# Performance work log

Measured on AMD Instinct MI355X. Metric: run time of the kernel, lower is better.

## Reference

```python
import jax, jax.numpy as jnp
import numpy as np

B, C, H = 16, 64, 128
W_SCALE = 0.05  # keep softmax logits in a sane range


def conv1x1_relu(x, w, b):
    # x: [B,C,H,W], w: [O,C] (1x1 conv kernel squeezed), b: [O]
    y = jnp.einsum('bchw,oc->bohw', x, w) + b[None, :, None, None]
    return jax.nn.relu(y)


def setup_inputs() -> dict:
    key = jax.random.key(0)
    ks = jax.random.split(key, 10)
    inp = {
        'x': jax.random.normal(ks[0], (B, C, H, H), dtype=jnp.float32),
        'att': jax.random.normal(ks[1], (B, C, H, H), dtype=jnp.float32),
    }
    for i in range(4):
        inp[f'w{i}'] = jax.random.normal(ks[2 + 2 * i], (C, C), dtype=jnp.float32) * W_SCALE
        inp[f'b{i}'] = jax.random.normal(ks[3 + 2 * i], (C,), dtype=jnp.float32) * W_SCALE
    return inp


def reference(x, att, w0, b0, w1, b1, w2, b2, w3, b3):
    bs, c, h, w = x.shape
    query = conv1x1_relu(x, w0, b0)    # [B,C,H,W]
    key_ = conv1x1_relu(att, w1, b1)   # [B,C,H,W]
    value = conv1x1_relu(x, w2, b2)    # [B,C,H,W]
    kt = jnp.swapaxes(key_, -2, -1)    # [B,C,W,H]
    attn1 = jax.nn.softmax(jnp.matmul(query, kt), axis=-1)  # [B,C,H,H]
    attn2 = jax.nn.softmax(jnp.matmul(kt, query), axis=-1)  # [B,C,W,W]
    out = jnp.matmul(jnp.matmul(attn1, value), attn2)       # [B,C,H,W]
    out = conv1x1_relu(out, w3, b3)
    return out.reshape(bs, -1, h, h)
```

## Files before the change

kernel.cpp:

```cpp
#include <hip/hip_runtime.h>
#include <stdint.h>

#define NB   16
#define NCH  64
#define HH   128
#define NPOS (HH*HH)

typedef short bf16x8 __attribute__((ext_vector_type(8)));
typedef float f32x4  __attribute__((ext_vector_type(4)));

__device__ __forceinline__ unsigned short f2bf(float f){
  unsigned int u = __float_as_uint(f);
  u += 0x7FFFu + ((u>>16)&1u);
  return (unsigned short)(u>>16);
}
__device__ __forceinline__ unsigned int pk2(float a, float b){
  return (unsigned int)f2bf(a) | ((unsigned int)f2bf(b)<<16);
}

__device__ __forceinline__ int swz(int row, int cb){
  return cb ^ (((row & 7) ^ ((row >> 3) & 7)) << 4);
}

__global__ __launch_bounds__(256) void rc_conv_in(
    const float* __restrict__ x, const float* __restrict__ att,
    const float* __restrict__ w0, const float* __restrict__ b0,
    const float* __restrict__ w1, const float* __restrict__ b1,
    const float* __restrict__ w2, const float* __restrict__ b2,
    unsigned short* __restrict__ Qb, unsigned short* __restrict__ Kb,
    unsigned short* __restrict__ Vb)
{
  __shared__ char smem[49664];
  char* Xs  = smem;
  char* WsA = smem + 32768;
  char* WsB = smem + 40960;
  float* biasA = (float*)(smem + 49152);
  float* biasB = (float*)(smem + 49408);

  const int tid = threadIdx.x;
  const int m  = blockIdx.z;
  const int b  = blockIdx.y;
  const int pblock = blockIdx.x * 256;
  const float* src = m ? att : x;
  const float* wA  = m ? w1 : w0;
  const float* bA  = m ? b1 : b0;

  {
    int o = tid >> 2, c0 = (tid & 3) * 16;
    const float4* wr = (const float4*)(wA + o*64 + c0);
    float4 f0 = wr[0], f1 = wr[1], f2v = wr[2], f3 = wr[3];
    uint4 pa, pb;
    pa.x = pk2(f0.x,f0.y);  pa.y = pk2(f0.z,f0.w);
    pa.z = pk2(f1.x,f1.y);  pa.w = pk2(f1.z,f1.w);
    pb.x = pk2(f2v.x,f2v.y); pb.y = pk2(f2v.z,f2v.w);
    pb.z = pk2(f3.x,f3.y);  pb.w = pk2(f3.z,f3.w);
    *(uint4*)(WsA + o*128 + swz(o, c0*2))      = pa;
    *(uint4*)(WsA + o*128 + swz(o, c0*2 + 16)) = pb;
    if (m == 0){
      const float4* wr2 = (const float4*)(w2 + o*64 + c0);
      float4 g0 = wr2[0], g1 = wr2[1], g2 = wr2[2], g3 = wr2[3];
      uint4 qa, qb;
      qa.x = pk2(g0.x,g0.y); qa.y = pk2(g0.z,g0.w);
      qa.z = pk2(g1.x,g1.y); qa.w = pk2(g1.z,g1.w);
      qb.x = pk2(g2.x,g2.y); qb.y = pk2(g2.z,g2.w);
      qb.z = pk2(g3.x,g3.y); qb.w = pk2(g3.z,g3.w);
      *(uint4*)(WsB + o*128 + swz(o, c0*2))      = qa;
      *(uint4*)(WsB + o*128 + swz(o, c0*2 + 16)) = qb;
    }
  }
  if (tid < 64){
    biasA[tid] = bA[tid];
    if (m == 0) biasB[tid] = b2[tid];
  }

  const float* S = src + (size_t)b*NCH*NPOS + pblock;
  #pragma unroll
  for (int it=0; it<4; ++it){
    int unit = tid + 256*it;
    int q  = unit >> 6;
    int p4 = (unit & 63) << 2;
    float4 r0 = *(const float4*)(S + (size_t)(4*q+0)*NPOS + p4);
    float4 r1 = *(const float4*)(S + (size_t)(4*q+1)*NPOS + p4);
    float4 r2 = *(const float4*)(S + (size_t)(4*q+2)*NPOS + p4);
    float4 r3 = *(const float4*)(S + (size_t)(4*q+3)*NPOS + p4);
    const float* c0 = (const float*)&r0;
    const float* c1 = (const float*)&r1;
    const float* c2 = (const float*)&r2;
    const float* c3 = (const float*)&r3;
    #pragma unroll
    for (int u=0; u<4; ++u){
      uint2 pk;
      pk.x = pk2(c0[u], c1[u]);
      pk.y = pk2(c2[u], c3[u]);
      *(uint2*)(Xs + (p4+u)*128 + swz(p4+u, q*8)) = pk;
    }
  }
  __syncthreads();

  const int w = tid>>6, l = tid&63, lq = l>>4, lm = l&15;
  bf16x8 aQ[2], aV[2] = {};
  {
    int orow = 16*w + lm;
    aQ[0] = *(const bf16x8*)(WsA + orow*128 + swz(orow,      lq*16));
    aQ[1] = *(const bf16x8*)(WsA + orow*128 + swz(orow, 64 + lq*16));
    if (m == 0){
      aV[0] = *(const bf16x8*)(WsB + orow*128 + swz(orow,      lq*16));
      aV[1] = *(const bf16x8*)(WsB + orow*128 + swz(orow, 64 + lq*16));
    }
  }
  float bQv[4], bVv[4];
  #pragma unroll
  for (int r4=0;r4<4;r4++){
    int o = 16*w + 4*lq + r4;
    bQv[r4] = biasA[o];
    bVv[r4] = (m==0) ? biasB[o] : 0.f;
  }
  unsigned short* dA = (m ? Kb : Qb) + (size_t)b*NCH*NPOS;
  unsigned short* dB = Vb + (size_t)b*NCH*NPOS;

  #pragma unroll
  for (int pt=0; pt<16; ++pt){
    int prow = pt*16 + lm;
    bf16x8 bx0 = *(const bf16x8*)(Xs + prow*128 + swz(prow,      lq*16));
    bf16x8 bx1 = *(const bf16x8*)(Xs + prow*128 + swz(prow, 64 + lq*16));
    f32x4 accQ = (f32x4){0.f,0.f,0.f,0.f};
    accQ = __builtin_amdgcn_mfma_f32_16x16x32_bf16(aQ[0], bx0, accQ, 0,0,0);
    accQ = __builtin_amdgcn_mfma_f32_16x16x32_bf16(aQ[1], bx1, accQ, 0,0,0);
    int p = pblock + pt*16 + lm;
    #pragma unroll
    for (int r4=0;r4<4;r4++){
      int o = 16*w + 4*lq + r4;
      dA[(size_t)o*NPOS + p] = f2bf(fmaxf(accQ[r4] + bQv[r4], 0.f));
    }
    if (m == 0){
      f32x4 accV = (f32x4){0.f,0.f,0.f,0.f};
      accV = __builtin_amdgcn_mfma_f32_16x16x32_bf16(aV[0], bx0, accV, 0,0,0);
      accV = __builtin_amdgcn_mfma_f32_16x16x32_bf16(aV[1], bx1, accV, 0,0,0);
      #pragma unroll
      for (int r4=0;r4<4;r4++){
        int o = 16*w + 4*lq + r4;
        dB[(size_t)o*NPOS + p] = f2bf(fmaxf(accV[r4] + bVv[r4], 0.f));
      }
    }
  }
}

__global__ __launch_bounds__(512) void rc_attention_mfma(
    const unsigned short* __restrict__ Qb, const unsigned short* __restrict__ Kb,
    const unsigned short* __restrict__ Vb, unsigned short* __restrict__ Pb)
{
  extern __shared__ char lds[];
  char* B0 = lds;
  char* B1 = lds + 32768;
  char* B2 = lds + 65536;
  char* B3 = lds + 98304;
  const int tid = threadIdx.x;
  const int l  = tid & 63;
  const int w  = tid >> 6;
  const int lq = l >> 4;
  const int lm = l & 15;
  const size_t gbase = (size_t)blockIdx.x * NPOS;

  uint4 vreg[4];
  #pragma unroll
  for (int i=0;i<4;i++)
    vreg[i] = *(const uint4*)(Vb + gbase + (size_t)(tid + 512*i)*8);

  #pragma unroll
  for (int i=0;i<4;i++){
    int e = (tid + 512*i)*8;
    int row = e >> 7, col = e & 127;
    uint4 q = *(const uint4*)(Qb + gbase + e);
    uint4 k = *(const uint4*)(Kb + gbase + e);
    *(uint4*)(B0 + row*256 + swz(row, col*2)) = q;
    *(uint4*)(B1 + row*256 + swz(row, col*2)) = k;
    unsigned int qd[4] = {q.x,q.y,q.z,q.w};
    unsigned int kd[4] = {k.x,k.y,k.z,k.w};
    #pragma unroll
    for (int u=0;u<8;u++){
      unsigned short qe = (unsigned short)(qd[u>>1] >> (16*(u&1)));
      unsigned short ke = (unsigned short)(kd[u>>1] >> (16*(u&1)));
      int tr = col + u;
      *(unsigned short*)(B2 + tr*256 + swz(tr, row*2)) = qe;
      *(unsigned short*)(B3 + tr*256 + swz(tr, row*2)) = ke;
    }
  }
  __syncthreads();

  f32x4 acc1[8];
  #pragma unroll
  for (int t=0;t<8;t++) acc1[t] = (f32x4){0.f,0.f,0.f,0.f};
  {
    bf16x8 bq[4];
    #pragma unroll
    for (int kk=0;kk<4;kk++){
      int r = 16*w + lm;
      bq[kk] = *(const bf16x8*)(B0 + r*256 + swz(r, kk*64 + lq*16));
    }
    #pragma unroll
    for (int kk=0;kk<4;kk++){
      #pragma unroll
      for (int jt=0;jt<8;jt++){
        int jr = jt*16 + lm;
        bf16x8 ak = *(const bf16x8*)(B1 + jr*256 + swz(jr, kk*64 + lq*16));
        acc1[jt] = __builtin_amdgcn_mfma_f32_16x16x32_bf16(ak, bq[kk], acc1[jt], 0,0,0);
      }
    }
  }
  unsigned int a1p[8][2];
  {
    float mx = -1e30f;
    #pragma unroll
    for (int t=0;t<8;t++)
      mx = fmaxf(mx, fmaxf(fmaxf(acc1[t][0], acc1[t][1]), fmaxf(acc1[t][2], acc1[t][3])));
    mx = fmaxf(mx, __shfl_xor(mx, 16));
    mx = fmaxf(mx, __shfl_xor(mx, 32));
    float sum = 0.f;
    #pragma unroll
    for (int t=0;t<8;t++){
      #pragma unroll
      for (int r4=0;r4<4;r4++){ float e = __expf(acc1[t][r4] - mx); acc1[t][r4] = e; sum += e; }
    }
    sum += __shfl_xor(sum, 16);
    sum += __shfl_xor(sum, 32);
    float inv = 1.f/sum;
    #pragma unroll
    for (int t=0;t<8;t++){
      a1p[t][0] = pk2(acc1[t][0]*inv, acc1[t][1]*inv);
      a1p[t][1] = pk2(acc1[t][2]*inv, acc1[t][3]*inv);
    }
  }

  f32x4 acc2[8];
  #pragma unroll
  for (int t=0;t<8;t++) acc2[t] = (f32x4){0.f,0.f,0.f,0.f};
  {
    bf16x8 akt[4];
    #pragma unroll
    for (int kk=0;kk<4;kk++){
      int ir = 16*w + lm;
      akt[kk] = *(const bf16x8*)(B3 + ir*256 + swz(ir, kk*64 + lq*16));
    }
    #pragma unroll
    for (int kk=0;kk<4;kk++){
      #pragma unroll
      for (int ct=0;ct<8;ct++){
        int jr = ct*16 + lm;
        bf16x8 bqt = *(const bf16x8*)(B2 + jr*256 + swz(jr, kk*64 + lq*16));
        acc2[ct] = __builtin_amdgcn_mfma_f32_16x16x32_bf16(akt[kk], bqt, acc2[ct], 0,0,0);
      }
    }
  }
  unsigned int a2p[8][2];
  {
    float m0=-1e30f, m1=-1e30f, m2=-1e30f, m3=-1e30f;
    #pragma unroll
    for (int t=0;t<8;t++){
      m0 = fmaxf(m0, acc2[t][0]); m1 = fmaxf(m1, acc2[t][1]);
      m2 = fmaxf(m2, acc2[t][2]); m3 = fmaxf(m3, acc2[t][3]);
    }
    #pragma unroll
    for (int d=1; d<16; d<<=1){
      m0 = fmaxf(m0, __shfl_xor(m0,d)); m1 = fmaxf(m1, __shfl_xor(m1,d));
      m2 = fmaxf(m2, __shfl_xor(m2,d)); m3 = fmaxf(m3, __shfl_xor(m3,d));
    }
    float s0=0.f, s1=0.f, s2=0.f, s3=0.f;
    #pragma unroll
    for (int t=0;t<8;t++){
      float e0 = __expf(acc2[t][0]-m0); acc2[t][0]=e0; s0 += e0;
      float e1 = __expf(acc2[t][1]-m1); acc2[t][1]=e1; s1 += e1;
      float e2 = __expf(acc2[t][2]-m2); acc2[t][2]=e2; s2 += e2;
      float e3 = __expf(acc2[t][3]-m3); acc2[t][3]=e3; s3 += e3;
    }
    #pragma unroll
    for (int d=1; d<16; d<<=1){
      s0 += __shfl_xor(s0,d); s1 += __shfl_xor(s1,d);
      s2 += __shfl_xor(s2,d); s3 += __shfl_xor(s3,d);
    }
    float i0=1.f/s0, i1=1.f/s1, i2=1.f/s2, i3=1.f/s3;
    #pragma unroll
    for (int t=0;t<8;t++){
      a2p[t][0] = pk2(acc2[t][0]*i0, acc2[t][1]*i1);
      a2p[t][1] = pk2(acc2[t][2]*i2, acc2[t][3]*i3);
    }
  }

  __syncthreads();

  {
    int r = 16*w + lm;
    #pragma unroll
    for (int t=0;t<8;t++)
      *(uint2*)(B3 + r*256 + swz(r, t*32 + lq*8)) = make_uint2(a1p[t][0], a1p[t][1]);
  }
  #pragma unroll
  for (int t=0;t<8;t++){
    int jr = t*16 + lm;
    *(uint2*)(B2 + jr*256 + swz(jr, 32*w + lq*8)) = make_uint2(a2p[t][0], a2p[t][1]);
  }
  #pragma unroll
  for (int i=0;i<4;i++){
    int e = (tid + 512*i)*8;
    int row = e>>7, col = e&127;
    unsigned int vd[4] = {vreg[i].x, vreg[i].y, vreg[i].z, vreg[i].w};
    #pragma unroll
    for (int u=0;u<8;u++){
      unsigned short ve = (unsigned short)(vd[u>>1] >> (16*(u&1)));
      int tr = col + u;
      *(unsigned short*)(B1 + tr*256 + swz(tr, row*2)) = ve;
    }
  }
  __syncthreads();

  f32x4 acc3[8];
  #pragma unroll
  for (int t=0;t<8;t++) acc3[t] = (f32x4){0.f,0.f,0.f,0.f};
  {
    bf16x8 av[4];
    #pragma unroll
    for (int kk=0;kk<4;kk++){
      int jr = 16*w + lm;
      av[kk] = *(const bf16x8*)(B1 + jr*256 + swz(jr, kk*64 + lq*16));
    }
    #pragma unroll
    for (int kk=0;kk<4;kk++){
      #pragma unroll
      for (int rt=0;rt<8;rt++){
        int rr = rt*16 + lm;
        bf16x8 ba = *(const bf16x8*)(B3 + rr*256 + swz(rr, kk*64 + lq*16));
        acc3[rt] = __builtin_amdgcn_mfma_f32_16x16x32_bf16(av[kk], ba, acc3[rt], 0,0,0);
      }
    }
  }
  #pragma unroll
  for (int rt=0;rt<8;rt++){
    int rr = rt*16 + lm;
    unsigned int p0 = pk2(acc3[rt][0], acc3[rt][1]);
    unsigned int p1 = pk2(acc3[rt][2], acc3[rt][3]);
    *(uint2*)(B0 + rr*256 + swz(rr, 32*w + lq*8)) = make_uint2(p0, p1);
  }
  __syncthreads();

  f32x4 acc4[8];
  #pragma unroll
  for (int t=0;t<8;t++) acc4[t] = (f32x4){0.f,0.f,0.f,0.f};
  {
    bf16x8 am[4];
    #pragma unroll
    for (int kk=0;kk<4;kk++){
      int rr = 16*w + lm;
      am[kk] = *(const bf16x8*)(B0 + rr*256 + swz(rr, kk*64 + lq*16));
    }
    #pragma unroll
    for (int kk=0;kk<4;kk++){
      #pragma unroll
      for (int ct=0;ct<8;ct++){
        int jr = ct*16 + lm;
        bf16x8 ba2 = *(const bf16x8*)(B2 + jr*256 + swz(jr, kk*64 + lq*16));
        acc4[ct] = __builtin_amdgcn_mfma_f32_16x16x32_bf16(am[kk], ba2, acc4[ct], 0,0,0);
      }
    }
  }
  unsigned short* pout = Pb + gbase;
  #pragma unroll
  for (int ct=0;ct<8;ct++){
    #pragma unroll
    for (int r4=0;r4<4;r4++){
      int rr = 16*w + lq*4 + r4;
      pout[rr*HH + ct*16 + lm] = f2bf(acc4[ct][r4]);
    }
  }
}

__global__ __launch_bounds__(256) void rc_conv_out(
    const unsigned short* __restrict__ Pb, const float* __restrict__ w3,
    const float* __restrict__ b3, float* __restrict__ out)
{
  __shared__ char smem[41216];
  char* Xs = smem;
  char* Ws = smem + 32768;
  float* bias = (float*)(smem + 40960);

  const int tid = threadIdx.x;
  const int b  = blockIdx.y;
  const int pblock = blockIdx.x * 256;

  {
    int o = tid >> 2, c0 = (tid & 3) * 16;
    const float4* wr = (const float4*)(w3 + o*64 + c0);
    float4 f0 = wr[0], f1 = wr[1], f2v = wr[2], f3 = wr[3];
    uint4 pa, pb;
    pa.x = pk2(f0.x,f0.y);  pa.y = pk2(f0.z,f0.w);
    pa.z = pk2(f1.x,f1.y);  pa.w = pk2(f1.z,f1.w);
    pb.x = pk2(f2v.x,f2v.y); pb.y = pk2(f2v.z,f2v.w);
    pb.z = pk2(f3.x,f3.y);  pb.w = pk2(f3.z,f3.w);
    *(uint4*)(Ws + o*128 + swz(o, c0*2))      = pa;
    *(uint4*)(Ws + o*128 + swz(o, c0*2 + 16)) = pb;
  }
  if (tid < 64) bias[tid] = b3[tid];

  const unsigned short* S = Pb + (size_t)b*NCH*NPOS + pblock;
  #pragma unroll
  for (int it=0; it<4; ++it){
    int unit = tid + 256*it;
    int q  = unit >> 6;
    int p4 = (unit & 63) << 2;
    uint2 r0 = *(const uint2*)(S + (size_t)(4*q+0)*NPOS + p4);
    uint2 r1 = *(const uint2*)(S + (size_t)(4*q+1)*NPOS + p4);
    uint2 r2 = *(const uint2*)(S + (size_t)(4*q+2)*NPOS + p4);
    uint2 r3 = *(const uint2*)(S + (size_t)(4*q+3)*NPOS + p4);
    const unsigned short* u0 = (const unsigned short*)&r0;
    const unsigned short* u1 = (const unsigned short*)&r1;
    const unsigned short* u2 = (const unsigned short*)&r2;
    const unsigned short* u3 = (const unsigned short*)&r3;
    #pragma unroll
    for (int u=0; u<4; ++u){
      uint2 pk;
      pk.x = (unsigned int)u0[u] | ((unsigned int)u1[u]<<16);
      pk.y = (unsigned int)u2[u] | ((unsigned int)u3[u]<<16);
      *(uint2*)(Xs + (p4+u)*128 + swz(p4+u, q*8)) = pk;
    }
  }
  __syncthreads();

  const int w = tid>>6, l = tid&63, lq = l>>4, lm = l&15;
  bf16x8 aW[2];
  {
    int orow = 16*w + lm;
    aW[0] = *(const bf16x8*)(Ws + orow*128 + swz(orow,      lq*16));
    aW[1] = *(const bf16x8*)(Ws + orow*128 + swz(orow, 64 + lq*16));
  }
  float bv[4];
  #pragma unroll
  for (int r4=0;r4<4;r4++) bv[r4] = bias[16*w + 4*lq + r4];

  float* dst = out + (size_t)b*NCH*NPOS;
  #pragma unroll
  for (int pt=0; pt<16; ++pt){
    int prow = pt*16 + lm;
    bf16x8 bx0 = *(const bf16x8*)(Xs + prow*128 + swz(prow,      lq*16));
    bf16x8 bx1 = *(const bf16x8*)(Xs + prow*128 + swz(prow, 64 + lq*16));
    f32x4 acc = (f32x4){0.f,0.f,0.f,0.f};
    acc = __builtin_amdgcn_mfma_f32_16x16x32_bf16(aW[0], bx0, acc, 0,0,0);
    acc = __builtin_amdgcn_mfma_f32_16x16x32_bf16(aW[1], bx1, acc, 0,0,0);
    int p = pblock + pt*16 + lm;
    #pragma unroll
    for (int r4=0;r4<4;r4++){
      int o = 16*w + 4*lq + r4;
      dst[(size_t)o*NPOS + p] = fmaxf(acc[r4] + bv[r4], 0.f);
    }
  }
}

extern "C" void kernel_launch(void* const* d_in, const int* in_sizes, int n_in,
                              void* d_out, int out_size, void* d_ws, size_t ws_size,
                              hipStream_t stream)
{
  const float* x   = (const float*)d_in[0];
  const float* att = (const float*)d_in[1];
  const float* w0  = (const float*)d_in[2]; const float* b0 = (const float*)d_in[3];
  const float* w1  = (const float*)d_in[4]; const float* b1 = (const float*)d_in[5];
  const float* w2  = (const float*)d_in[6]; const float* b2 = (const float*)d_in[7];
  const float* w3  = (const float*)d_in[8]; const float* b3 = (const float*)d_in[9];

  const size_t NM = (size_t)NB*NCH*NPOS;
  unsigned short* Qb = (unsigned short*)d_ws;
  unsigned short* Kb = Qb + NM;
  unsigned short* Vb = Kb + NM;
  unsigned short* Pb = Vb + NM;
  float* out = (float*)d_out;

  (void)hipFuncSetAttribute((const void*)rc_attention_mfma,
                            hipFuncAttributeMaxDynamicSharedMemorySize, 131072);

  rc_conv_in<<<dim3(64, NB, 2), 256, 0, stream>>>(x, att, w0,b0, w1,b1, w2,b2,
                                                  Qb, Kb, Vb);

  rc_attention_mfma<<<dim3(NB*NCH), 512, 131072, stream>>>(Qb, Kb, Vb, Pb);

  rc_conv_out<<<dim3(64, NB), 256, 0, stream>>>(Pb, w3, b3, out);
}
```

Before: 125.5 us.

## Halve conv tile size, batch loads, and stage conv_in outputs through LDS

Both 1x1 conv kernels now handle 128 positions per block instead of 256 and launch twice as many blocks. They set launch-bound occupancy hints and issue all global loads before converting into LDS. In conv_in, results are accumulated for all tiles, then transposed through swizzled LDS so each thread writes 16-byte vectors instead of scattered 2-byte stores. This targets poor store coalescing and low occupancy, at the cost of extra barriers and more accumulator registers.

```diff
diff --git a/kernel.cpp b/kernel.cpp
--- a/kernel.cpp
+++ b/kernel.cpp
@@ -22,7 +22,7 @@
   return cb ^ (((row & 7) ^ ((row >> 3) & 7)) << 4);
 }
 
-__global__ __launch_bounds__(256) void rc_conv_in(
+__global__ __launch_bounds__(256, 4) void rc_conv_in(
     const float* __restrict__ x, const float* __restrict__ att,
     const float* __restrict__ w0, const float* __restrict__ b0,
     const float* __restrict__ w1, const float* __restrict__ b1,
@@ -30,17 +30,17 @@
     unsigned short* __restrict__ Qb, unsigned short* __restrict__ Kb,
     unsigned short* __restrict__ Vb)
 {
-  __shared__ char smem[49664];
+  __shared__ char smem[33280];
   char* Xs  = smem;
-  char* WsA = smem + 32768;
-  char* WsB = smem + 40960;
-  float* biasA = (float*)(smem + 49152);
-  float* biasB = (float*)(smem + 49408);
+  char* WsA = smem + 16384;
+  char* WsB = smem + 24576;
+  float* biasA = (float*)(smem + 32768);
+  float* biasB = (float*)(smem + 33024);
 
   const int tid = threadIdx.x;
   const int m  = blockIdx.z;
   const int b  = blockIdx.y;
-  const int pblock = blockIdx.x * 256;
+  const int pblock = blockIdx.x * 128;
   const float* src = m ? att : x;
   const float* wA  = m ? w1 : w0;
   const float* bA  = m ? b1 : b0;
@@ -74,19 +74,25 @@
   }
 
   const float* S = src + (size_t)b*NCH*NPOS + pblock;
-  #pragma unroll
-  for (int it=0; it<4; ++it){
-    int unit = tid + 256*it;
-    int q  = unit >> 6;
-    int p4 = (unit & 63) << 2;
-    float4 r0 = *(const float4*)(S + (size_t)(4*q+0)*NPOS + p4);
-    float4 r1 = *(const float4*)(S + (size_t)(4*q+1)*NPOS + p4);
-    float4 r2 = *(const float4*)(S + (size_t)(4*q+2)*NPOS + p4);
-    float4 r3 = *(const float4*)(S + (size_t)(4*q+3)*NPOS + p4);
-    const float* c0 = (const float*)&r0;
-    const float* c1 = (const float*)&r1;
-    const float* c2 = (const float*)&r2;
-    const float* c3 = (const float*)&r3;
+  float4 xr[2][4];
+  #pragma unroll
+  for (int g=0; g<2; ++g){
+    int unit = tid + 256*g;
+    int q  = unit >> 5;
+    int p4 = (unit & 31) << 2;
+    #pragma unroll
+    for (int j=0;j<4;j++)
+      xr[g][j] = *(const float4*)(S + (size_t)(4*q+j)*NPOS + p4);
+  }
+  #pragma unroll
+  for (int g=0; g<2; ++g){
+    int unit = tid + 256*g;
+    int q  = unit >> 5;
+    int p4 = (unit & 31) << 2;
+    const float* c0 = (const float*)&xr[g][0];
+    const float* c1 = (const float*)&xr[g][1];
+    const float* c2 = (const float*)&xr[g][2];
+    const float* c3 = (const float*)&xr[g][3];
     #pragma unroll
     for (int u=0; u<4; ++u){
       uint2 pk;
@@ -115,32 +121,69 @@
     bQv[r4] = biasA[o];
     bVv[r4] = (m==0) ? biasB[o] : 0.f;
   }
-  unsigned short* dA = (m ? Kb : Qb) + (size_t)b*NCH*NPOS;
-  unsigned short* dB = Vb + (size_t)b*NCH*NPOS;
-
-  #pragma unroll
-  for (int pt=0; pt<16; ++pt){
+
+  f32x4 accQ[8], accV[8];
+  #pragma unroll
+  for (int pt=0;pt<8;pt++){ accQ[pt]=(f32x4){0,0,0,0}; accV[pt]=(f32x4){0,0,0,0}; }
+  #pragma unroll
+  for (int pt=0; pt<8; ++pt){
     int prow = pt*16 + lm;
     bf16x8 bx0 = *(const bf16x8*)(Xs + prow*128 + swz(prow,      lq*16));
     bf16x8 bx1 = *(const bf16x8*)(Xs + prow*128 + swz(prow, 64 + lq*16));
-    f32x4 accQ = (f32x4){0.f,0.f,0.f,0.f};
-    accQ = __builtin_amdgcn_mfma_f32_16x16x32_bf16(aQ[0], bx0, accQ, 0,0,0);
-    accQ = __builtin_amdgcn_mfma_f32_16x16x32_bf16(aQ[1], bx1, accQ, 0,0,0);
-    int p = pblock + pt*16 + lm;
+    accQ[pt] = __builtin_amdgcn_mfma_f32_16x16x32_bf16(aQ[0], bx0, accQ[pt], 0,0,0);
+    accQ[pt] = __builtin_amdgcn_mfma_f32_16x16x32_bf16(aQ[1], bx1, accQ[pt], 0,0,0);
+    if (m == 0){
+      accV[pt] = __builtin_amdgcn_mfma_f32_16x16x32_bf16(aV[0], bx0, accV[pt], 0,0,0);
+      accV[pt] = __builtin_amdgcn_mfma_f32_16x16x32_bf16(aV[1], bx1, accV[pt], 0,0,0);
+    }
+  }
+
+  unsigned short* dA = (m ? Kb : Qb) + (size_t)b*NCH*NPOS;
+  unsigned short* dB = Vb + (size_t)b*NCH*NPOS;
+  const int skw = 32*((4*w + lq) & 7);
+
+  __syncthreads();
+  #pragma unroll
+  for (int pt=0; pt<8; ++pt){
     #pragma unroll
     for (int r4=0;r4<4;r4++){
       int o = 16*w + 4*lq + r4;
-      dA[(size_t)o*NPOS + p] = f2bf(fmaxf(accQ[r4] + bQv[r4], 0.f));
-    }
-    if (m == 0){
-      f32x4 accV = (f32x4){0.f,0.f,0.f,0.f};
-      accV = __builtin_amdgcn_mfma_f32_16x16x32_bf16(aV[0], bx0, accV, 0,0,0);
-      accV = __builtin_amdgcn_mfma_f32_16x16x32_bf16(aV[1], bx1, accV, 0,0,0);
+      int p = pt*16 + lm;
+      *(unsigned short*)(Xs + o*256 + ((2*p + skw) & 255)) =
+          f2bf(fmaxf(accQ[pt][r4] + bQv[r4], 0.f));
+    }
+  }
+  __syncthreads();
+  {
+    int o = tid >> 2, jj = tid & 3;
+    int sk2 = 32*((o>>2)&7);
+    #pragma unroll
+    for (int i=0;i<4;i++){
+      int j = i*4 + jj;
+      uint4 v = *(const uint4*)(Xs + o*256 + ((j*16 + sk2) & 255));
+      *(uint4*)(dA + (size_t)o*NPOS + pblock + j*8) = v;
+    }
+  }
+  if (m == 0){
+    __syncthreads();
+    #pragma unroll
+    for (int pt=0; pt<8; ++pt){
       #pragma unroll
       for (int r4=0;r4<4;r4++){
         int o = 16*w + 4*lq + r4;
-        dB[(size_t)o*NPOS + p] = f2bf(fmaxf(accV[r4] + bVv[r4], 0.f));
+        int p = pt*16 + lm;
+        *(unsigned short*)(Xs + o*256 + ((2*p + skw) & 255)) =
+            f2bf(fmaxf(accV[pt][r4] + bVv[r4], 0.f));
       }
+    }
+    __syncthreads();
+    int o = tid >> 2, jj = tid & 3;
+    int sk2 = 32*((o>>2)&7);
+    #pragma unroll
+    for (int i=0;i<4;i++){
+      int j = i*4 + jj;
+      uint4 v = *(const uint4*)(Xs + o*256 + ((j*16 + sk2) & 255));
+      *(uint4*)(dB + (size_t)o*NPOS + pblock + j*8) = v;
     }
   }
 }
@@ -372,18 +415,18 @@
   }
 }
 
-__global__ __launch_bounds__(256) void rc_conv_out(
+__global__ __launch_bounds__(256, 6) void rc_conv_out(
     const unsigned short* __restrict__ Pb, const float* __restrict__ w3,
     const float* __restrict__ b3, float* __restrict__ out)
 {
-  __shared__ char smem[41216];
+  __shared__ char smem[24832];
   char* Xs = smem;
-  char* Ws = smem + 32768;
-  float* bias = (float*)(smem + 40960);
+  char* Ws = smem + 16384;
+  float* bias = (float*)(smem + 24576);
 
   const int tid = threadIdx.x;
   const int b  = blockIdx.y;
-  const int pblock = blockIdx.x * 256;
+  const int pblock = blockIdx.x * 128;
 
   {
     int o = tid >> 2, c0 = (tid & 3) * 16;
@@ -400,24 +443,30 @@
   if (tid < 64) bias[tid] = b3[tid];
 
   const unsigned short* S = Pb + (size_t)b*NCH*NPOS + pblock;
-  #pragma unroll
-  for (int it=0; it<4; ++it){
-    int unit = tid + 256*it;
-    int q  = unit >> 6;
-    int p4 = (unit & 63) << 2;
-    uint2 r0 = *(const uint2*)(S + (size_t)(4*q+0)*NPOS + p4);
-    uint2 r1 = *(const uint2*)(S + (size_t)(4*q+1)*NPOS + p4);
-    uint2 r2 = *(const uint2*)(S + (size_t)(4*q+2)*NPOS + p4);
-    uint2 r3 = *(const uint2*)(S + (size_t)(4*q+3)*NPOS + p4);
-    const unsigned short* u0 = (const unsigned short*)&r0;
-    const unsigned short* u1 = (const unsigned short*)&r1;
-    const unsigned short* u2 = (const unsigned short*)&r2;
-    const unsigned short* u3 = (const unsigned short*)&r3;
+  uint2 pr[2][4];
+  #pragma unroll
+  for (int g=0; g<2; ++g){
+    int unit = tid + 256*g;
+    int q  = unit >> 5;
+    int p4 = (unit & 31) << 2;
+    #pragma unroll
+    for (int j=0;j<4;j++)
+      pr[g][j] = *(const uint2*)(S + (size_t)(4*q+j)*NPOS + p4);
+  }
+  #pragma unroll
+  for (int g=0; g<2; ++g){
+    int unit = tid + 256*g;
+    int q  = unit >> 5;
+    int p4 = (unit & 31) << 2;
+    const unsigned short* e0 = (const unsigned short*)&pr[g][0];
+    const unsigned short* e1 = (const unsigned short*)&pr[g][1];
+    const unsigned short* e2 = (const unsigned short*)&pr[g][2];
+    const unsigned short* e3 = (const unsigned short*)&pr[g][3];
     #pragma unroll
     for (int u=0; u<4; ++u){
       uint2 pk;
-      pk.x = (unsigned int)u0[u] | ((unsigned int)u1[u]<<16);
-      pk.y = (unsigned int)u2[u] | ((unsigned int)u3[u]<<16);
+      pk.x = (unsigned int)e0[u] | ((unsigned int)e1[u]<<16);
+      pk.y = (unsigned int)e2[u] | ((unsigned int)e3[u]<<16);
       *(uint2*)(Xs + (p4+u)*128 + swz(p4+u, q*8)) = pk;
     }
   }
@@ -436,7 +485,7 @@
 
   float* dst = out + (size_t)b*NCH*NPOS;
   #pragma unroll
-  for (int pt=0; pt<16; ++pt){
+  for (int pt=0; pt<8; ++pt){
     int prow = pt*16 + lm;
     bf16x8 bx0 = *(const bf16x8*)(Xs + prow*128 + swz(prow,      lq*16));
     bf16x8 bx1 = *(const bf16x8*)(Xs + prow*128 + swz(prow, 64 + lq*16));
@@ -473,10 +522,10 @@
   (void)hipFuncSetAttribute((const void*)rc_attention_mfma,
                             hipFuncAttributeMaxDynamicSharedMemorySize, 131072);
 
-  rc_conv_in<<<dim3(64, NB, 2), 256, 0, stream>>>(x, att, w0,b0, w1,b1, w2,b2,
-                                                  Qb, Kb, Vb);
+  rc_conv_in<<<dim3(128, NB, 2), 256, 0, stream>>>(x, att, w0,b0, w1,b1, w2,b2,
+                                                   Qb, Kb, Vb);
 
   rc_attention_mfma<<<dim3(NB*NCH), 512, 131072, stream>>>(Qb, Kb, Vb, Pb);
 
-  rc_conv_out<<<dim3(64, NB), 256, 0, stream>>>(Pb, w3, b3, out);
-}
+  rc_conv_out<<<dim3(128, NB), 256, 0, stream>>>(Pb, w3, b3, out);
+}
```

After: 118.9 us (median of 2 runs). 5.3% less time.
